# Kernel optimization log

Measured on AMD Instinct MI355X. Metric: run time of the kernel, lower is better.

The kernel has to match this reference:

```python
import jax, jax.numpy as jnp
import numpy as np


def setup_inputs() -> dict:
    key = jax.random.key(0)
    k1, k2, k3 = jax.random.split(key, 3)
    B, C, L, D = 2, 8, 256, 128
    start_hidden = jax.random.normal(k1, (B, C, L, D), dtype=jnp.float32)
    end_hidden = jax.random.normal(k2, (B, C, L, D), dtype=jnp.float32)
    # nn.Parameter initialized uniform_(-0.1, 0.1)
    v = jax.random.uniform(k3, (D,), dtype=jnp.float32, minval=-0.1, maxval=0.1)
    return {"start_hidden": start_hidden, "end_hidden": end_hidden, "v": v}


def reference(start_hidden, end_hidden, v):
    # start_hidden: [B, C, L, D], end_hidden: [B, C, L, D], v: [D]
    # additive pairwise scoring: tanh(s_i + e_j) . v  for every (i, j) span
    add_hidden = jnp.tanh(start_hidden[:, :, :, None, :] + end_hidden[:, :, None, :, :])  # [B,C,L,L,D]
    res = jnp.einsum('bcnmd,d->bcnm', add_hidden, v)  # [B, C, L, L]
    span_ner_mat_tensor = jnp.transpose(res, (0, 2, 3, 1))  # [B, L, L, C]
    return span_ner_mat_tensor
```

## Files before the change

kernel.cpp:

```cpp
#include <hip/hip_runtime.h>


#define LDIM 256
#define DDIM 128
#define DPAD 132

__global__ __launch_bounds__(256, 4) void span_tanh_dot_kernel(
    const float* __restrict__ start_h,
    const float* __restrict__ end_h,
    const float* __restrict__ v,
    float* __restrict__ out,
    int C)
{
    __shared__ float s_t[32][DPAD];
    __shared__ float e_t[32][DPAD];
    __shared__ float s_vsum;

    const int bc = blockIdx.z;
    const int i0 = blockIdx.y * 32;
    const int j0 = blockIdx.x * 32;
    const int tx = threadIdx.x;
    const int ty = threadIdx.y;
    const int g  = threadIdx.z;
    const int t  = ty * 8 + tx;
    const int tid = g * 64 + t;

    const float K = 2.8853900817779268f;

    const float* sg = start_h + ((size_t)bc * LDIM + i0) * DDIM;
    const float* eg = end_h   + ((size_t)bc * LDIM + j0) * DDIM;

    #pragma unroll
    for (int k = 0; k < 4; ++k) {
        const int idx = tid + k * 256;
        const int r  = idx >> 5;
        const int c4 = (idx & 31) << 2;
        float4 a = *(const float4*)(sg + r * DDIM + c4);
        a.x = __builtin_amdgcn_exp2f(K * a.x);
        a.y = __builtin_amdgcn_exp2f(K * a.y);
        a.z = __builtin_amdgcn_exp2f(K * a.z);
        a.w = __builtin_amdgcn_exp2f(K * a.w);
        *(float4*)(&s_t[r][c4]) = a;
        float4 b = *(const float4*)(eg + r * DDIM + c4);
        b.x = __builtin_amdgcn_exp2f(K * b.x);
        b.y = __builtin_amdgcn_exp2f(K * b.y);
        b.z = __builtin_amdgcn_exp2f(K * b.z);
        b.w = __builtin_amdgcn_exp2f(K * b.w);
        *(float4*)(&e_t[r][c4]) = b;
    }

    if (g == 0) {
        float2 vv = *(const float2*)(v + 2 * t);
        float p = vv.x + vv.y;
        #pragma unroll
        for (int off = 1; off < 64; off <<= 1) p += __shfl_xor(p, off);
        if (t == 0) s_vsum = p;
    }
    __syncthreads();

    float acc[4][4];
    #pragma unroll
    for (int a = 0; a < 4; ++a)
        #pragma unroll
        for (int b = 0; b < 4; ++b) acc[a][b] = 0.0f;

    const int dbase = g * 32;

    #pragma unroll 2
    for (int it = 0; it < 8; ++it) {
        const int d = dbase + it * 4;
        float4 S[4], E[4];
        #pragma unroll
        for (int k = 0; k < 4; ++k) {
            S[k] = *(const float4*)(&s_t[ty + 8 * k][d]);
            E[k] = *(const float4*)(&e_t[tx + 8 * k][d]);
        }
        const float4 vv = *(const float4*)(v + d);

        #pragma unroll
        for (int a = 0; a < 4; ++a) {
            #pragma unroll
            for (int b = 0; b < 4; ++b) {
                float q0 = fmaf(S[a].x, E[b].x, 1.0f);
                float q1 = fmaf(S[a].y, E[b].y, 1.0f);
                float q2 = fmaf(S[a].z, E[b].z, 1.0f);
                float q3 = fmaf(S[a].w, E[b].w, 1.0f);
                float ab = q0 * q1, cd = q2 * q3;
                float n01 = fmaf(vv.x, q1, vv.y * q0);
                float n23 = fmaf(vv.z, q3, vv.w * q2);
                float N = fmaf(n01, cd, n23 * ab);
                float r = __builtin_amdgcn_rcpf(ab * cd);
                acc[a][b] = fmaf(N, r, acc[a][b]);
            }
        }
    }

    __syncthreads();
    float4* redv = (float4*)(&s_t[0][0]);
    #pragma unroll
    for (int a = 0; a < 4; ++a) {
        float4 row; row.x = acc[a][0]; row.y = acc[a][1];
        row.z = acc[a][2]; row.w = acc[a][3];
        redv[(g * 64 + t) * 4 + ((a + t) & 3)] = row;
    }
    __syncthreads();

    float4 sum = redv[t * 4 + ((g + t) & 3)];
    #pragma unroll
    for (int src = 1; src < 4; ++src) {
        float4 r4 = redv[(src * 64 + t) * 4 + ((g + t) & 3)];
        sum.x += r4.x; sum.y += r4.y; sum.z += r4.z; sum.w += r4.w;
    }

    const int b_ = bc / C;
    const int c_ = bc - b_ * C;
    const float Sv = s_vsum;
    const int i = i0 + ty + 8 * g;
    const size_t rowbase = (((size_t)b_ * LDIM + i) * LDIM) * C + c_;
    out[rowbase + (size_t)(j0 + tx     ) * C] = fmaf(-2.f, sum.x, Sv);
    out[rowbase + (size_t)(j0 + tx +  8) * C] = fmaf(-2.f, sum.y, Sv);
    out[rowbase + (size_t)(j0 + tx + 16) * C] = fmaf(-2.f, sum.z, Sv);
    out[rowbase + (size_t)(j0 + tx + 24) * C] = fmaf(-2.f, sum.w, Sv);
}

extern "C" void kernel_launch(void* const* d_in, const int* in_sizes, int n_in,
                              void* d_out, int out_size, void* d_ws, size_t ws_size,
                              hipStream_t stream) {
    const float* start_h = (const float*)d_in[0];
    const float* end_h   = (const float*)d_in[1];
    const float* v       = (const float*)d_in[2];
    float* out = (float*)d_out;

    const int BC = in_sizes[0] / (LDIM * DDIM);
    const int C  = 8;

    dim3 grid(LDIM / 32, LDIM / 32, BC);
    dim3 block(8, 8, 4);
    span_tanh_dot_kernel<<<grid, block, 0, stream>>>(start_h, end_h, v, out, C);
}
```

Before: 19.77 us.

## Store exp-transformed tiles as bf16 in LDS and use a tree reduction

Rounds the exp2-transformed start/end tiles to bf16 and stores them in shared memory. This halves LDS footprint and read bandwidth in the inner loop, but adds unpack instructions and loses precision. The inner loop is now fully unrolled. The 4-group cross-slice reduction becomes a two-stage tree, with group 0 alone writing all 16 outputs per thread, and the vsum is kept in registers instead of shared memory.

```diff
diff --git a/kernel.cpp b/kernel.cpp
--- a/kernel.cpp
+++ b/kernel.cpp
@@ -3,7 +3,18 @@
 
 #define LDIM 256
 #define DDIM 128
-#define DPAD 132
+#define DPADH 136
+
+__device__ __forceinline__ unsigned bf1(float x) {
+    unsigned u = __float_as_uint(x);
+    u += 0x7FFFu + ((u >> 16) & 1u);
+    return u >> 16;
+}
+__device__ __forceinline__ unsigned pack2(float x, float y) {
+    return bf1(x) | (bf1(y) << 16);
+}
+__device__ __forceinline__ float lo16(unsigned u) { return __uint_as_float(u << 16); }
+__device__ __forceinline__ float hi16(unsigned u) { return __uint_as_float(u & 0xFFFF0000u); }
 
 __global__ __launch_bounds__(256, 4) void span_tanh_dot_kernel(
     const float* __restrict__ start_h,
@@ -12,9 +23,9 @@
     float* __restrict__ out,
     int C)
 {
-    __shared__ float s_t[32][DPAD];
-    __shared__ float e_t[32][DPAD];
-    __shared__ float s_vsum;
+    __shared__ unsigned short s_t[32][DPADH];
+    __shared__ unsigned short e_t[32][DPADH];
+    __shared__ float4 red[2 * 64 * 4];
 
     const int bc = blockIdx.z;
     const int i0 = blockIdx.y * 32;
@@ -31,32 +42,39 @@
     const float* eg = end_h   + ((size_t)bc * LDIM + j0) * DDIM;
 
     #pragma unroll
-    for (int k = 0; k < 4; ++k) {
+    for (int k = 0; k < 2; ++k) {
         const int idx = tid + k * 256;
-        const int r  = idx >> 5;
-        const int c4 = (idx & 31) << 2;
-        float4 a = *(const float4*)(sg + r * DDIM + c4);
-        a.x = __builtin_amdgcn_exp2f(K * a.x);
-        a.y = __builtin_amdgcn_exp2f(K * a.y);
-        a.z = __builtin_amdgcn_exp2f(K * a.z);
-        a.w = __builtin_amdgcn_exp2f(K * a.w);
-        *(float4*)(&s_t[r][c4]) = a;
-        float4 b = *(const float4*)(eg + r * DDIM + c4);
-        b.x = __builtin_amdgcn_exp2f(K * b.x);
-        b.y = __builtin_amdgcn_exp2f(K * b.y);
-        b.z = __builtin_amdgcn_exp2f(K * b.z);
-        b.w = __builtin_amdgcn_exp2f(K * b.w);
-        *(float4*)(&e_t[r][c4]) = b;
+        const int r  = idx >> 4;
+        const int c8 = (idx & 15) << 3;
+        float4 a0 = *(const float4*)(sg + r * DDIM + c8);
+        float4 a1 = *(const float4*)(sg + r * DDIM + c8 + 4);
+        uint4 pa;
+        pa.x = pack2(__builtin_amdgcn_exp2f(K * a0.x), __builtin_amdgcn_exp2f(K * a0.y));
+        pa.y = pack2(__builtin_amdgcn_exp2f(K * a0.z), __builtin_amdgcn_exp2f(K * a0.w));
+        pa.z = pack2(__builtin_amdgcn_exp2f(K * a1.x), __builtin_amdgcn_exp2f(K * a1.y));
+        pa.w = pack2(__builtin_amdgcn_exp2f(K * a1.z), __builtin_amdgcn_exp2f(K * a1.w));
+        *(uint4*)(&s_t[r][c8]) = pa;
+        float4 b0 = *(const float4*)(eg + r * DDIM + c8);
+        float4 b1 = *(const float4*)(eg + r * DDIM + c8 + 4);
+        uint4 pb;
+        pb.x = pack2(__builtin_amdgcn_exp2f(K * b0.x), __builtin_amdgcn_exp2f(K * b0.y));
+        pb.y = pack2(__builtin_amdgcn_exp2f(K * b0.z), __builtin_amdgcn_exp2f(K * b0.w));
+        pb.z = pack2(__builtin_amdgcn_exp2f(K * b1.x), __builtin_amdgcn_exp2f(K * b1.y));
+        pb.w = pack2(__builtin_amdgcn_exp2f(K * b1.z), __builtin_amdgcn_exp2f(K * b1.w));
+        *(uint4*)(&e_t[r][c8]) = pb;
     }
 
+    float Sv = 0.0f;
     if (g == 0) {
         float2 vv = *(const float2*)(v + 2 * t);
-        float p = vv.x + vv.y;
+        Sv = vv.x + vv.y;
         #pragma unroll
-        for (int off = 1; off < 64; off <<= 1) p += __shfl_xor(p, off);
-        if (t == 0) s_vsum = p;
+        for (int off = 1; off < 64; off <<= 1) Sv += __shfl_xor(Sv, off);
     }
     __syncthreads();
+
+    const int gb = __builtin_amdgcn_readfirstlane(g);
+    const int dbase = gb * 32;
 
     float acc[4][4];
     #pragma unroll
@@ -64,30 +82,36 @@
         #pragma unroll
         for (int b = 0; b < 4; ++b) acc[a][b] = 0.0f;
 
-    const int dbase = g * 32;
-
-    #pragma unroll 2
+    #pragma unroll
     for (int it = 0; it < 8; ++it) {
         const int d = dbase + it * 4;
-        float4 S[4], E[4];
+        uint2 Sr[4], Er[4];
         #pragma unroll
         for (int k = 0; k < 4; ++k) {
-            S[k] = *(const float4*)(&s_t[ty + 8 * k][d]);
-            E[k] = *(const float4*)(&e_t[tx + 8 * k][d]);
+            Sr[k] = *(const uint2*)(&s_t[ty + 8 * k][d]);
+            Er[k] = *(const uint2*)(&e_t[tx + 8 * k][d]);
         }
-        const float4 vv = *(const float4*)(v + d);
+        float Sf[4][4], Ef[4][4];
+        #pragma unroll
+        for (int k = 0; k < 4; ++k) {
+            Sf[k][0] = lo16(Sr[k].x); Sf[k][1] = hi16(Sr[k].x);
+            Sf[k][2] = lo16(Sr[k].y); Sf[k][3] = hi16(Sr[k].y);
+            Ef[k][0] = lo16(Er[k].x); Ef[k][1] = hi16(Er[k].x);
+            Ef[k][2] = lo16(Er[k].y); Ef[k][3] = hi16(Er[k].y);
+        }
+        const float v0 = v[d], v1 = v[d + 1], v2 = v[d + 2], v3 = v[d + 3];
 
         #pragma unroll
         for (int a = 0; a < 4; ++a) {
             #pragma unroll
             for (int b = 0; b < 4; ++b) {
-                float q0 = fmaf(S[a].x, E[b].x, 1.0f);
-                float q1 = fmaf(S[a].y, E[b].y, 1.0f);
-                float q2 = fmaf(S[a].z, E[b].z, 1.0f);
-                float q3 = fmaf(S[a].w, E[b].w, 1.0f);
+                float q0 = fmaf(Sf[a][0], Ef[b][0], 1.0f);
+                float q1 = fmaf(Sf[a][1], Ef[b][1], 1.0f);
+                float q2 = fmaf(Sf[a][2], Ef[b][2], 1.0f);
+                float q3 = fmaf(Sf[a][3], Ef[b][3], 1.0f);
                 float ab = q0 * q1, cd = q2 * q3;
-                float n01 = fmaf(vv.x, q1, vv.y * q0);
-                float n23 = fmaf(vv.z, q3, vv.w * q2);
+                float n01 = fmaf(v0, q1, v1 * q0);
+                float n23 = fmaf(v2, q3, v3 * q2);
                 float N = fmaf(n01, cd, n23 * ab);
                 float r = __builtin_amdgcn_rcpf(ab * cd);
                 acc[a][b] = fmaf(N, r, acc[a][b]);
@@ -95,32 +119,43 @@
         }
     }
 
-    __syncthreads();
-    float4* redv = (float4*)(&s_t[0][0]);
-    #pragma unroll
-    for (int a = 0; a < 4; ++a) {
-        float4 row; row.x = acc[a][0]; row.y = acc[a][1];
-        row.z = acc[a][2]; row.w = acc[a][3];
-        redv[(g * 64 + t) * 4 + ((a + t) & 3)] = row;
+    if (g >= 2) {
+        #pragma unroll
+        for (int a = 0; a < 4; ++a)
+            red[((g - 2) * 64 + t) * 4 + a] =
+                make_float4(acc[a][0], acc[a][1], acc[a][2], acc[a][3]);
     }
     __syncthreads();
-
-    float4 sum = redv[t * 4 + ((g + t) & 3)];
-    #pragma unroll
-    for (int src = 1; src < 4; ++src) {
-        float4 r4 = redv[(src * 64 + t) * 4 + ((g + t) & 3)];
-        sum.x += r4.x; sum.y += r4.y; sum.z += r4.z; sum.w += r4.w;
+    if (g < 2) {
+        #pragma unroll
+        for (int a = 0; a < 4; ++a) {
+            float4 p = red[(g * 64 + t) * 4 + a];
+            acc[a][0] += p.x; acc[a][1] += p.y; acc[a][2] += p.z; acc[a][3] += p.w;
+        }
     }
-
-    const int b_ = bc / C;
-    const int c_ = bc - b_ * C;
-    const float Sv = s_vsum;
-    const int i = i0 + ty + 8 * g;
-    const size_t rowbase = (((size_t)b_ * LDIM + i) * LDIM) * C + c_;
-    out[rowbase + (size_t)(j0 + tx     ) * C] = fmaf(-2.f, sum.x, Sv);
-    out[rowbase + (size_t)(j0 + tx +  8) * C] = fmaf(-2.f, sum.y, Sv);
-    out[rowbase + (size_t)(j0 + tx + 16) * C] = fmaf(-2.f, sum.z, Sv);
-    out[rowbase + (size_t)(j0 + tx + 24) * C] = fmaf(-2.f, sum.w, Sv);
+    __syncthreads();
+    if (g == 1) {
+        #pragma unroll
+        for (int a = 0; a < 4; ++a)
+            red[t * 4 + a] = make_float4(acc[a][0], acc[a][1], acc[a][2], acc[a][3]);
+    }
+    __syncthreads();
+    if (g == 0) {
+        const int b_ = bc / C;
+        const int c_ = bc - b_ * C;
+        #pragma unroll
+        for (int a = 0; a < 4; ++a) {
+            float4 p = red[t * 4 + a];
+            acc[a][0] += p.x; acc[a][1] += p.y; acc[a][2] += p.z; acc[a][3] += p.w;
+            const int i = i0 + ty + 8 * a;
+            const size_t rowbase = (((size_t)b_ * LDIM + i) * LDIM) * C + c_;
+            #pragma unroll
+            for (int b2 = 0; b2 < 4; ++b2) {
+                const int j = j0 + tx + 8 * b2;
+                out[rowbase + (size_t)j * C] = fmaf(-2.0f, acc[a][b2], Sv);
+            }
+        }
+    }
 }
 
 extern "C" void kernel_launch(void* const* d_in, const int* in_sizes, int n_in,
```

Result: slower. 69.17 us (+249.9%).
